# Kernel tuning notes

Measured on AMD Instinct MI355X. Metric: run time of the kernel, lower is better.

Reference implementation:

```python
import jax, jax.numpy as jnp
import numpy as np

N_NODES = 100000
N_EDGES = 1600000
DIM_IN = 128
DIM_OUT = 128


def setup_inputs() -> dict:
    key = jax.random.key(0)
    k_x, k_e, k_w = jax.random.split(key, 3)
    x = jax.random.normal(k_x, (N_NODES, DIM_IN), dtype=jnp.float32)
    edge_index = jax.random.randint(k_e, (2, N_EDGES), 0, N_NODES, dtype=jnp.int64)
    # Glorot-uniform weight like PyG's GCNConv linear layer, stored [d_in, d_out]
    limit = np.sqrt(6.0 / (DIM_IN + DIM_OUT)).astype(np.float32)
    W = jax.random.uniform(k_w, (DIM_IN, DIM_OUT), dtype=jnp.float32, minval=-limit, maxval=limit)
    return {"x": x, "edge_index": edge_index, "W": W}


def reference(x, edge_index, W):
    # PyG GCNConv (bias=False): out = D^{-1/2} (A + I) D^{-1/2} (x @ W)
    N = x.shape[0]
    x_proj = x @ W  # [N, d_out]
    loop = jnp.arange(N, dtype=edge_index.dtype)
    src = jnp.concatenate([edge_index[0], loop])  # message sources (row)
    dst = jnp.concatenate([edge_index[1], loop])  # aggregation targets (col)
    # degree counted at target nodes (edge weight = 1), incl. self loops
    deg = jax.ops.segment_sum(jnp.ones(src.shape, dtype=x.dtype), dst, num_segments=N)
    dis = jnp.where(deg > 0, jax.lax.rsqrt(deg), 0.0)
    norm = dis[src] * dis[dst]  # [E+N]
    msgs = x_proj[src] * norm[:, None]  # [E+N, d_out] gather + scale
    return jax.ops.segment_sum(msgs, dst, num_segments=N)  # scatter-add
```

## Files before the change

### kernel.cpp

```cpp
#include <hip/hip_runtime.h>
#include <hip/hip_bf16.h>

#define DIM 128
#define PCH 2048

typedef __attribute__((ext_vector_type(8))) short bf16x8;
typedef __attribute__((ext_vector_type(4))) float f32x4;

__device__ __forceinline__ float bfu_lo(unsigned u) { return __uint_as_float(u << 16); }
__device__ __forceinline__ float bfu_hi(unsigned u) { return __uint_as_float(u & 0xffff0000u); }
__device__ __forceinline__ unsigned short f2bf(float f) {
    unsigned u = __float_as_uint(f);
    u += 0x7fffu + ((u >> 16) & 1u);
    return (unsigned short)(u >> 16);
}

__device__ __forceinline__ int edge_at(const void* ei, int idx64, long long pos) {
    return idx64 ? (int)__builtin_nontemporal_load((const long long*)ei + pos)
                 : __builtin_nontemporal_load((const int*)ei + pos);
}

__device__ __forceinline__ int detect_idx64(const void* ei, int E, unsigned* s_or, int* s_flag) {
    const unsigned* ei_w = (const unsigned*)ei;
    int t = threadIdx.x;
    unsigned o = 0;
    int lim = (E < 4096) ? E : 4096;
    for (int k = t; k < lim; k += 256) o |= ei_w[2 * k + 1];
    s_or[t] = o;
    __syncthreads();
    for (int s = 128; s > 0; s >>= 1) {
        if (t < s) s_or[t] |= s_or[t + s];
        __syncthreads();
    }
    if (t == 0) *s_flag = (s_or[0] == 0u) ? 1 : 0;
    __syncthreads();
    return *s_flag;
}

__global__ __launch_bounds__(256) void hist_detect(const void* ei, unsigned* bcnt,
                                                   int* flags, int E, int shift) {
    __shared__ unsigned s_h[512];
    __shared__ unsigned s_or[256];
    __shared__ int s_flag;
    int t = threadIdx.x;
    for (int i = t; i < 512; i += 256) s_h[i] = 0u;
    int idx64 = detect_idx64(ei, E, s_or, &s_flag);
    if (blockIdx.x == 0 && t == 0) flags[0] = idx64;
    long long stride = (long long)gridDim.x * 256;
    for (long long e = (long long)blockIdx.x * 256 + t; e < E; e += stride) {
        int d = edge_at(ei, idx64, (long long)E + e);
        atomicAdd(&s_h[d >> shift], 1u);
    }
    __syncthreads();
    for (int i = t; i < 512; i += 256)
        if (s_h[i]) atomicAdd(&bcnt[i], s_h[i]);
}

__global__ __launch_bounds__(256) void partition(const void* ei, const int* __restrict__ flags,
                                                 const unsigned* __restrict__ bcnt,
                                                 unsigned* bcur0, unsigned* pout,
                                                 int E, int B, int shift) {
    __shared__ unsigned s_hist[512], s_off[512], s_gbase[512], s_pref[512], s_bbase[512];
    __shared__ unsigned wsum[4];
    __shared__ unsigned d_arr[PCH], s_arr[PCH];
    int t = threadIdx.x;
    long long base = (long long)blockIdx.x * PCH;
    for (int i = t; i < 512; i += 256) { s_hist[i] = 0u; s_off[i] = 0u; }
    int idx64 = flags[0];

    {
        unsigned v0 = bcnt[2 * t], v1 = bcnt[2 * t + 1];
        unsigned ps = v0 + v1;
        unsigned s = ps;
        int lane = t & 63;
#pragma unroll
        for (int off = 1; off < 64; off <<= 1) {
            unsigned u = __shfl_up(s, off, 64);
            if (lane >= off) s += u;
        }
        int w = t >> 6;
        if (lane == 63) wsum[w] = s;
        __syncthreads();
        unsigned woff = 0;
        for (int j = 0; j < w; j++) woff += wsum[j];
        unsigned excl = woff + s - ps;
        s_bbase[2 * t] = excl;
        s_bbase[2 * t + 1] = excl + v0;
    }
    __syncthreads();

    int d_[PCH / 256], s_[PCH / 256];
#pragma unroll
    for (int j = 0; j < PCH / 256; j++) {
        long long e = base + j * 256 + t;
        if (e < E) {
            d_[j] = edge_at(ei, idx64, (long long)E + e);
            s_[j] = edge_at(ei, idx64, e);
            atomicAdd(&s_hist[d_[j] >> shift], 1u);
        } else d_[j] = -1;
    }
    __syncthreads();

    {
        unsigned v0 = s_hist[2 * t], v1 = s_hist[2 * t + 1];
        unsigned ps = v0 + v1;
        unsigned s = ps;
        int lane = t & 63;
#pragma unroll
        for (int off = 1; off < 64; off <<= 1) {
            unsigned u = __shfl_up(s, off, 64);
            if (lane >= off) s += u;
        }
        int w = t >> 6;
        if (lane == 63) wsum[w] = s;
        __syncthreads();
        unsigned woff = 0;
        for (int j = 0; j < w; j++) woff += wsum[j];
        unsigned excl = woff + s - ps;
        s_pref[2 * t] = excl;
        s_pref[2 * t + 1] = excl + v0;
    }
    __syncthreads();

    for (int i = t; i < B; i += 256)
        if (s_hist[i]) s_gbase[i] = s_bbase[i] + atomicAdd(&bcur0[i], s_hist[i]);
#pragma unroll
    for (int j = 0; j < PCH / 256; j++)
        if (d_[j] >= 0) {
            int b = d_[j] >> shift;
            unsigned p = s_pref[b] + atomicAdd(&s_off[b], 1u);
            d_arr[p] = (unsigned)d_[j];
            s_arr[p] = (unsigned)s_[j];
        }
    __syncthreads();
    long long rem = (long long)E - base;
    unsigned tot = (rem < PCH) ? (unsigned)rem : (unsigned)PCH;
    unsigned msk = (1u << shift) - 1u;
    for (unsigned i = t; i < tot; i += 256) {
        unsigned d = d_arr[i];
        int b = (int)(d >> shift);
        unsigned packed = ((d & msk) << (32 - shift)) | s_arr[i];
        pout[s_gbase[b] + (i - s_pref[b])] = packed;
    }
}

__global__ __launch_bounds__(256) void build_csr(const unsigned* __restrict__ pairs,
                                                 const unsigned* __restrict__ bcnt,
                                                 unsigned* deg, unsigned* row_start,
                                                 float* dis, int* col_src,
                                                 int N, int shift) {
    __shared__ unsigned cnt[512], cur[512], pref[512];
    __shared__ unsigned s_bb[513];
    __shared__ unsigned wsum[4];
    int b = blockIdx.x, t = threadIdx.x;
    int npb = 1 << shift;
    if (npb > 512) npb = 512;
    int nodeLo = b << shift;
    unsigned smask = (1u << (32 - shift)) - 1u;

    {
        unsigned v0 = bcnt[2 * t], v1 = bcnt[2 * t + 1];
        unsigned ps = v0 + v1;
        unsigned s = ps;
        int lane = t & 63;
#pragma unroll
        for (int off = 1; off < 64; off <<= 1) {
            unsigned u = __shfl_up(s, off, 64);
            if (lane >= off) s += u;
        }
        int w = t >> 6;
        if (lane == 63) wsum[w] = s;
        __syncthreads();
        unsigned woff = 0;
        for (int j = 0; j < w; j++) woff += wsum[j];
        unsigned excl = woff + s - ps;
        s_bb[2 * t] = excl;
        s_bb[2 * t + 1] = excl + v0;
        if (t == 255) s_bb[512] = excl + ps;
    }
    __syncthreads();
    unsigned lo = s_bb[b], hi = s_bb[b + 1];

    for (int i = t; i < npb; i += 256) cnt[i] = 0u;
    __syncthreads();
    for (unsigned e = lo + t; e < hi; e += 256) {
        unsigned p = pairs[e];
        atomicAdd(&cnt[p >> (32 - shift)], 1u);
    }
    __syncthreads();
    unsigned v0 = (2 * t < npb) ? cnt[2 * t] : 0u;
    unsigned v1 = (2 * t + 1 < npb) ? cnt[2 * t + 1] : 0u;
    unsigned ps = v0 + v1;
    unsigned s = ps;
    int lane = t & 63;
#pragma unroll
    for (int off = 1; off < 64; off <<= 1) {
        unsigned u = __shfl_up(s, off, 64);
        if (lane >= off) s += u;
    }
    int w = t >> 6;
    if (lane == 63) wsum[w] = s;
    __syncthreads();
    unsigned woff = 0;
    for (int j = 0; j < w; j++) woff += wsum[j];
    unsigned excl = woff + s - ps;
    if (2 * t < npb) pref[2 * t] = excl;
    if (2 * t + 1 < npb) pref[2 * t + 1] = excl + v0;
    __syncthreads();
    for (int i = t; i < npb; i += 256) {
        int node = nodeLo + i;
        unsigned rs = lo + pref[i];
        if (node < N) {
            unsigned c = cnt[i];
            deg[node] = c;
            row_start[node] = rs;
            dis[node] = rsqrtf((float)c + 1.0f);
        }
        cur[i] = rs;
    }
    __syncthreads();
    for (unsigned e = lo + t; e < hi; e += 256) {
        unsigned p = pairs[e];
        unsigned dlow = p >> (32 - shift);
        unsigned pos = atomicAdd(&cur[dlow], 1u);
        col_src[pos] = (int)(p & smask);
    }
}

__global__ __launch_bounds__(256) void gemm_xw(const float* __restrict__ x,
                                               const float* __restrict__ W,
                                               const float* __restrict__ dis,
                                               unsigned short* __restrict__ xps, int N) {
    __shared__ unsigned short wt[128 * 136];
    int tid = threadIdx.x;
    for (int idx = tid; idx < DIM * DIM; idx += 256) {
        int k = idx >> 7, n = idx & 127;
        wt[n * 136 + k] = f2bf(W[idx]);
    }
    __syncthreads();

    int wv = tid >> 6, lane = tid & 63;
    int l15 = lane & 15, quad = lane >> 4;
    int rowBase = blockIdx.x * 128 + wv * 32;

    f32x4 acc[2][8];
#pragma unroll
    for (int mt = 0; mt < 2; mt++)
#pragma unroll
        for (int nt = 0; nt < 8; nt++)
            acc[mt][nt] = (f32x4){0.f, 0.f, 0.f, 0.f};

#pragma unroll
    for (int k0 = 0; k0 < DIM; k0 += 32) {
        bf16x8 aa[2], bb[8];
#pragma unroll
        for (int mt = 0; mt < 2; mt++) {
            int r = rowBase + mt * 16 + l15;
            if (r > N - 1) r = N - 1;
            const float* xf = x + (size_t)r * DIM + k0 + quad * 8;
            float4 u0 = ((const float4*)xf)[0];
            float4 u1 = ((const float4*)xf)[1];
            bf16x8 a;
            a[0] = (short)f2bf(u0.x); a[1] = (short)f2bf(u0.y);
            a[2] = (short)f2bf(u0.z); a[3] = (short)f2bf(u0.w);
            a[4] = (short)f2bf(u1.x); a[5] = (short)f2bf(u1.y);
            a[6] = (short)f2bf(u1.z); a[7] = (short)f2bf(u1.w);
            aa[mt] = a;
        }
#pragma unroll
        for (int nt = 0; nt < 8; nt++)
            bb[nt] = *(const bf16x8*)(wt + (nt * 16 + l15) * 136 + k0 + quad * 8);
#pragma unroll
        for (int mt = 0; mt < 2; mt++)
#pragma unroll
            for (int nt = 0; nt < 8; nt++)
                acc[mt][nt] = __builtin_amdgcn_mfma_f32_16x16x32_bf16(bb[nt], aa[mt], acc[mt][nt], 0, 0, 0);
    }

#pragma unroll
    for (int mt = 0; mt < 2; mt++) {
        int r = rowBase + mt * 16 + l15;
        if (r < N) {
            float sc = dis[r];
#pragma unroll
            for (int nt = 0; nt < 8; nt++) {
                int c0 = nt * 16 + quad * 4;
                ushort4 o;
                o.x = f2bf(acc[mt][nt][0] * sc);
                o.y = f2bf(acc[mt][nt][1] * sc);
                o.z = f2bf(acc[mt][nt][2] * sc);
                o.w = f2bf(acc[mt][nt][3] * sc);
                *(ushort4*)(xps + (size_t)r * DIM + c0) = o;
            }
        }
    }
}

__global__ __launch_bounds__(256) void aggregate(const unsigned short* __restrict__ xps,
                                                 const unsigned* __restrict__ row_start,
                                                 const unsigned* __restrict__ deg,
                                                 const float* __restrict__ dis,
                                                 const int* __restrict__ col_src,
                                                 float* __restrict__ out, int N) {
    int wid = (int)((blockIdx.x * 256 + threadIdx.x) >> 6);
    if (wid >= N) return;
    int lane = threadIdx.x & 63;
    int grp = lane >> 4, lin = lane & 15;
    const uint4* xp4 = (const uint4*)xps;

    float acc[8];
#pragma unroll
    for (int j = 0; j < 8; j++) acc[j] = 0.f;

    unsigned rs = row_start[wid];
    unsigned cnt = deg[wid];
    unsigned tot = cnt + 1;

    for (unsigned base = 0; base < tot; base += 64) {
        unsigned slot = base + (unsigned)lane;
        int idx = (slot < cnt) ? col_src[rs + slot] : wid;
        unsigned rem = tot - base; if (rem > 64) rem = 64;
        for (unsigned q = 0; q * 8 < rem; q++) {
            unsigned sl0 = q * 8 + (unsigned)grp;
            unsigned sl1 = sl0 + 4;
            int s0 = __shfl(idx, (int)sl0, 64);
            int s1 = __shfl(idx, (int)sl1, 64);
            float m0 = (sl0 < rem) ? 1.f : 0.f;
            float m1 = (sl1 < rem) ? 1.f : 0.f;
            uint4 v0 = xp4[(size_t)s0 * 16 + lin];
            uint4 v1 = xp4[(size_t)s1 * 16 + lin];
            acc[0] = fmaf(bfu_lo(v0.x), m0, acc[0]);
            acc[1] = fmaf(bfu_hi(v0.x), m0, acc[1]);
            acc[2] = fmaf(bfu_lo(v0.y), m0, acc[2]);
            acc[3] = fmaf(bfu_hi(v0.y), m0, acc[3]);
            acc[4] = fmaf(bfu_lo(v0.z), m0, acc[4]);
            acc[5] = fmaf(bfu_hi(v0.z), m0, acc[5]);
            acc[6] = fmaf(bfu_lo(v0.w), m0, acc[6]);
            acc[7] = fmaf(bfu_hi(v0.w), m0, acc[7]);
            acc[0] = fmaf(bfu_lo(v1.x), m1, acc[0]);
            acc[1] = fmaf(bfu_hi(v1.x), m1, acc[1]);
            acc[2] = fmaf(bfu_lo(v1.y), m1, acc[2]);
            acc[3] = fmaf(bfu_hi(v1.y), m1, acc[3]);
            acc[4] = fmaf(bfu_lo(v1.z), m1, acc[4]);
            acc[5] = fmaf(bfu_hi(v1.z), m1, acc[5]);
            acc[6] = fmaf(bfu_lo(v1.w), m1, acc[6]);
            acc[7] = fmaf(bfu_hi(v1.w), m1, acc[7]);
        }
    }

#pragma unroll
    for (int j = 0; j < 8; j++) {
        acc[j] += __shfl_xor(acc[j], 16, 64);
        acc[j] += __shfl_xor(acc[j], 32, 64);
    }

    float di = dis[wid];
    if (grp < 2) {
        int jb = (grp & 1) * 4;
        float4 o;
        o.x = acc[jb + 0] * di;
        o.y = acc[jb + 1] * di;
        o.z = acc[jb + 2] * di;
        o.w = acc[jb + 3] * di;
        *(float4*)(out + (size_t)wid * DIM + lin * 8 + jb) = o;
    }
}

extern "C" void kernel_launch(void* const* d_in, const int* in_sizes, int n_in,
                              void* d_out, int out_size, void* d_ws, size_t ws_size,
                              hipStream_t stream) {
    const int N = in_sizes[0] / DIM;
    const int E = in_sizes[1] / 2;
    const float* x = (const float*)d_in[0];
    const void* ei = d_in[1];
    const float* W = (const float*)d_in[2];
    float* out = (float*)d_out;

    int shift = 8;
    while ((((long long)N + (1LL << shift) - 1) >> shift) > 512 && shift < 9) shift++;
    int B = (int)(((long long)N + (1LL << shift) - 1) >> shift);

    char* wsp = (char*)d_ws;
    size_t off = 0;
    auto alloc = [&](size_t b) { void* p = wsp + off; off += (b + 255) & ~(size_t)255; return p; };
    unsigned* bcnt       = (unsigned*)alloc(4096);
    unsigned* bcur0      = bcnt + 512;
    int*      flags      = (int*)alloc(256);
    unsigned* deg        = (unsigned*)alloc((size_t)N * 4);
    unsigned* row_start  = (unsigned*)alloc((size_t)N * 4);
    float*    dis        = (float*)alloc((size_t)N * 4);
    int*      col_src    = (int*)alloc((size_t)E * 4);
    unsigned short* xps  = (unsigned short*)alloc((size_t)N * DIM * 2);

    unsigned* pairs = (unsigned*)xps;
    if ((size_t)E * 4 > (size_t)N * DIM * 2 && off + (size_t)E * 4 <= ws_size)
        pairs = (unsigned*)alloc((size_t)E * 4);

    hipMemsetAsync(bcnt, 0, 4096, stream);
    hist_detect<<<512, 256, 0, stream>>>(ei, bcnt, flags, E, shift);
    partition<<<(E + PCH - 1) / PCH, 256, 0, stream>>>(ei, flags, bcnt, bcur0, pairs, E, B, shift);
    build_csr<<<B, 256, 0, stream>>>(pairs, bcnt, deg, row_start, dis, col_src, N, shift);
    gemm_xw<<<(N + 127) / 128, 256, 0, stream>>>(x, W, dis, xps, N);
    aggregate<<<(N + 3) / 4, 256, 0, stream>>>(xps, row_start, deg, dis, col_src, out, N);
}
```

Measured before the change: 244.9 us.

## Switch CSR build to coarse 2048-node partition with fine per-block filtering

The edge partition now bins destinations into 64 coarse buckets of 2048 nodes instead of up to 512 buckets of 256 nodes, with a larger 4096-edge chunk per partition block. This cuts the scattered global writes in partition to few contiguous runs. build_csr then launches one block per 256-node fine bucket; each block scans its whole coarse bucket (8x redundant reads of pairs), keeps only its own edges and stages them in LDS before scattering into col_src, falling back to a rescan if more than 8192 match. The packing hardcodes 21 bits for the source id, so it assumes N is below 2^21.

```diff
diff --git a/kernel.cpp b/kernel.cpp
--- a/kernel.cpp
+++ b/kernel.cpp
@@ -2,7 +2,11 @@
 #include <hip/hip_bf16.h>
 
 #define DIM 128
-#define PCH 2048
+#define PCH 4096
+#define CAP 8192
+#define SHIFT_F 8
+#define SHIFT_C 11
+#define FPC 8
 
 typedef __attribute__((ext_vector_type(8))) short bf16x8;
 typedef __attribute__((ext_vector_type(4))) float f32x4;
@@ -38,54 +42,43 @@
 }
 
 __global__ __launch_bounds__(256) void hist_detect(const void* ei, unsigned* bcnt,
-                                                   int* flags, int E, int shift) {
-    __shared__ unsigned s_h[512];
+                                                   int* flags, int E) {
+    __shared__ unsigned s_h[64];
     __shared__ unsigned s_or[256];
     __shared__ int s_flag;
     int t = threadIdx.x;
-    for (int i = t; i < 512; i += 256) s_h[i] = 0u;
+    if (t < 64) s_h[t] = 0u;
     int idx64 = detect_idx64(ei, E, s_or, &s_flag);
     if (blockIdx.x == 0 && t == 0) flags[0] = idx64;
     long long stride = (long long)gridDim.x * 256;
     for (long long e = (long long)blockIdx.x * 256 + t; e < E; e += stride) {
         int d = edge_at(ei, idx64, (long long)E + e);
-        atomicAdd(&s_h[d >> shift], 1u);
-    }
-    __syncthreads();
-    for (int i = t; i < 512; i += 256)
-        if (s_h[i]) atomicAdd(&bcnt[i], s_h[i]);
+        atomicAdd(&s_h[d >> SHIFT_C], 1u);
+    }
+    __syncthreads();
+    if (t < 64 && s_h[t]) atomicAdd(&bcnt[t], s_h[t]);
 }
 
 __global__ __launch_bounds__(256) void partition(const void* ei, const int* __restrict__ flags,
                                                  const unsigned* __restrict__ bcnt,
                                                  unsigned* bcur0, unsigned* pout,
-                                                 int E, int B, int shift) {
-    __shared__ unsigned s_hist[512], s_off[512], s_gbase[512], s_pref[512], s_bbase[512];
-    __shared__ unsigned wsum[4];
+                                                 int E, int Bc) {
+    __shared__ unsigned s_hist[64], s_off[64], s_gbase[64], s_pref[64], s_bbase[64];
     __shared__ unsigned d_arr[PCH], s_arr[PCH];
     int t = threadIdx.x;
     long long base = (long long)blockIdx.x * PCH;
-    for (int i = t; i < 512; i += 256) { s_hist[i] = 0u; s_off[i] = 0u; }
+    if (t < 64) { s_hist[t] = 0u; s_off[t] = 0u; }
     int idx64 = flags[0];
 
-    {
-        unsigned v0 = bcnt[2 * t], v1 = bcnt[2 * t + 1];
-        unsigned ps = v0 + v1;
-        unsigned s = ps;
-        int lane = t & 63;
+    if (t < 64) {
+        unsigned v = (t < Bc) ? bcnt[t] : 0u;
+        unsigned s = v;
 #pragma unroll
         for (int off = 1; off < 64; off <<= 1) {
             unsigned u = __shfl_up(s, off, 64);
-            if (lane >= off) s += u;
-        }
-        int w = t >> 6;
-        if (lane == 63) wsum[w] = s;
-        __syncthreads();
-        unsigned woff = 0;
-        for (int j = 0; j < w; j++) woff += wsum[j];
-        unsigned excl = woff + s - ps;
-        s_bbase[2 * t] = excl;
-        s_bbase[2 * t + 1] = excl + v0;
+            if (t >= off) s += u;
+        }
+        s_bbase[t] = s - v;
     }
     __syncthreads();
 
@@ -96,38 +89,29 @@
         if (e < E) {
             d_[j] = edge_at(ei, idx64, (long long)E + e);
             s_[j] = edge_at(ei, idx64, e);
-            atomicAdd(&s_hist[d_[j] >> shift], 1u);
+            atomicAdd(&s_hist[d_[j] >> SHIFT_C], 1u);
         } else d_[j] = -1;
     }
     __syncthreads();
 
-    {
-        unsigned v0 = s_hist[2 * t], v1 = s_hist[2 * t + 1];
-        unsigned ps = v0 + v1;
-        unsigned s = ps;
-        int lane = t & 63;
+    if (t < 64) {
+        unsigned v = s_hist[t];
+        unsigned s = v;
 #pragma unroll
         for (int off = 1; off < 64; off <<= 1) {
             unsigned u = __shfl_up(s, off, 64);
-            if (lane >= off) s += u;
-        }
-        int w = t >> 6;
-        if (lane == 63) wsum[w] = s;
-        __syncthreads();
-        unsigned woff = 0;
-        for (int j = 0; j < w; j++) woff += wsum[j];
-        unsigned excl = woff + s - ps;
-        s_pref[2 * t] = excl;
-        s_pref[2 * t + 1] = excl + v0;
-    }
-    __syncthreads();
-
-    for (int i = t; i < B; i += 256)
-        if (s_hist[i]) s_gbase[i] = s_bbase[i] + atomicAdd(&bcur0[i], s_hist[i]);
+            if (t >= off) s += u;
+        }
+        s_pref[t] = s - v;
+    }
+    __syncthreads();
+
+    if (t < Bc && s_hist[t])
+        s_gbase[t] = s_bbase[t] + atomicAdd(&bcur0[t], s_hist[t]);
 #pragma unroll
     for (int j = 0; j < PCH / 256; j++)
         if (d_[j] >= 0) {
-            int b = d_[j] >> shift;
+            int b = d_[j] >> SHIFT_C;
             unsigned p = s_pref[b] + atomicAdd(&s_off[b], 1u);
             d_arr[p] = (unsigned)d_[j];
             s_arr[p] = (unsigned)s_[j];
@@ -135,12 +119,12 @@
     __syncthreads();
     long long rem = (long long)E - base;
     unsigned tot = (rem < PCH) ? (unsigned)rem : (unsigned)PCH;
-    unsigned msk = (1u << shift) - 1u;
+    unsigned msk = (1u << SHIFT_C) - 1u;
     for (unsigned i = t; i < tot; i += 256) {
         unsigned d = d_arr[i];
-        int b = (int)(d >> shift);
-        unsigned packed = ((d & msk) << (32 - shift)) | s_arr[i];
-        pout[s_gbase[b] + (i - s_pref[b])] = packed;
+        int b = (int)(d >> SHIFT_C);
+        unsigned pk = ((d & msk) << 21) | s_arr[i];
+        pout[s_gbase[b] + (i - s_pref[b])] = pk;
     }
 }
 
@@ -148,51 +132,61 @@
                                                  const unsigned* __restrict__ bcnt,
                                                  unsigned* deg, unsigned* row_start,
                                                  float* dis, int* col_src,
-                                                 int N, int shift) {
-    __shared__ unsigned cnt[512], cur[512], pref[512];
-    __shared__ unsigned s_bb[513];
+                                                 int N, int Bc) {
+    __shared__ unsigned cnt[256], cur[256], pref[256];
+    __shared__ unsigned s_cb[65];
+    __shared__ unsigned s_sib[FPC];
+    __shared__ unsigned s_scnt;
+    __shared__ unsigned stage[CAP];
     __shared__ unsigned wsum[4];
     int b = blockIdx.x, t = threadIdx.x;
-    int npb = 1 << shift;
-    if (npb > 512) npb = 512;
-    int nodeLo = b << shift;
-    unsigned smask = (1u << (32 - shift)) - 1u;
-
-    {
-        unsigned v0 = bcnt[2 * t], v1 = bcnt[2 * t + 1];
-        unsigned ps = v0 + v1;
-        unsigned s = ps;
-        int lane = t & 63;
+    int g = b >> 3, myfine = b & (FPC - 1);
+    int lane = t & 63;
+
+    if (t < 64) {
+        unsigned v = (t < Bc) ? bcnt[t] : 0u;
+        unsigned s = v;
 #pragma unroll
         for (int off = 1; off < 64; off <<= 1) {
             unsigned u = __shfl_up(s, off, 64);
-            if (lane >= off) s += u;
-        }
-        int w = t >> 6;
-        if (lane == 63) wsum[w] = s;
-        __syncthreads();
-        unsigned woff = 0;
-        for (int j = 0; j < w; j++) woff += wsum[j];
-        unsigned excl = woff + s - ps;
-        s_bb[2 * t] = excl;
-        s_bb[2 * t + 1] = excl + v0;
-        if (t == 255) s_bb[512] = excl + ps;
-    }
-    __syncthreads();
-    unsigned lo = s_bb[b], hi = s_bb[b + 1];
-
-    for (int i = t; i < npb; i += 256) cnt[i] = 0u;
-    __syncthreads();
-    for (unsigned e = lo + t; e < hi; e += 256) {
-        unsigned p = pairs[e];
-        atomicAdd(&cnt[p >> (32 - shift)], 1u);
-    }
-    __syncthreads();
-    unsigned v0 = (2 * t < npb) ? cnt[2 * t] : 0u;
-    unsigned v1 = (2 * t + 1 < npb) ? cnt[2 * t + 1] : 0u;
-    unsigned ps = v0 + v1;
-    unsigned s = ps;
-    int lane = t & 63;
+            if (t >= off) s += u;
+        }
+        s_cb[t] = s - v;
+        if (t == 63) s_cb[64] = s;
+    }
+    cnt[t] = 0u;
+    if (t < FPC) s_sib[t] = 0u;
+    if (t == 0) s_scnt = 0u;
+    __syncthreads();
+    unsigned lo = s_cb[g], hi = (g + 1 < 64) ? s_cb[g + 1] : s_cb[64];
+
+    unsigned iters = (hi - lo + 255u) >> 8;
+    for (unsigned it = 0; it < iters; ++it) {
+        unsigned e = lo + it * 256u + (unsigned)t;
+        bool valid = e < hi;
+        unsigned p = valid ? pairs[e] : 0u;
+        unsigned dlow = p >> 21;
+        int sib = (int)(dlow >> SHIFT_F);
+        bool keep = valid && (sib == myfine);
+        if (valid) atomicAdd(&s_sib[sib], 1u);
+        if (keep) atomicAdd(&cnt[dlow & 255u], 1u);
+        unsigned long long mask = __ballot(keep);
+        if (mask) {
+            int leader = (int)__ffsll((long long)mask) - 1;
+            int rank = (int)__popcll(mask & ((1ull << lane) - 1ull));
+            unsigned basew = 0;
+            if (lane == leader) basew = atomicAdd(&s_scnt, (unsigned)__popcll(mask));
+            basew = (unsigned)__shfl((int)basew, leader, 64);
+            if (keep && basew + (unsigned)rank < CAP) stage[basew + rank] = p;
+        }
+    }
+    __syncthreads();
+
+    unsigned fbase = lo;
+    for (int j = 0; j < myfine; j++) fbase += s_sib[j];
+
+    unsigned v = cnt[t];
+    unsigned s = v;
 #pragma unroll
     for (int off = 1; off < 64; off <<= 1) {
         unsigned u = __shfl_up(s, off, 64);
@@ -203,27 +197,37 @@
     __syncthreads();
     unsigned woff = 0;
     for (int j = 0; j < w; j++) woff += wsum[j];
-    unsigned excl = woff + s - ps;
-    if (2 * t < npb) pref[2 * t] = excl;
-    if (2 * t + 1 < npb) pref[2 * t + 1] = excl + v0;
-    __syncthreads();
-    for (int i = t; i < npb; i += 256) {
-        int node = nodeLo + i;
-        unsigned rs = lo + pref[i];
-        if (node < N) {
-            unsigned c = cnt[i];
-            deg[node] = c;
-            row_start[node] = rs;
-            dis[node] = rsqrtf((float)c + 1.0f);
-        }
-        cur[i] = rs;
-    }
-    __syncthreads();
-    for (unsigned e = lo + t; e < hi; e += 256) {
-        unsigned p = pairs[e];
-        unsigned dlow = p >> (32 - shift);
-        unsigned pos = atomicAdd(&cur[dlow], 1u);
-        col_src[pos] = (int)(p & smask);
+    pref[t] = woff + s - v;
+    __syncthreads();
+
+    int node = (b << SHIFT_F) + t;
+    unsigned rs = fbase + pref[t];
+    if (node < N) {
+        unsigned c = cnt[t];
+        deg[node] = c;
+        row_start[node] = rs;
+        dis[node] = rsqrtf((float)c + 1.0f);
+    }
+    cur[t] = rs;
+    __syncthreads();
+
+    unsigned total = s_scnt;
+    if (total <= CAP) {
+        for (unsigned k = t; k < total; k += 256) {
+            unsigned p = stage[k];
+            unsigned n8 = (p >> 21) & 255u;
+            unsigned pos = atomicAdd(&cur[n8], 1u);
+            col_src[pos] = (int)(p & 0x1FFFFFu);
+        }
+    } else {
+        for (unsigned e = lo + t; e < hi; e += 256) {
+            unsigned p = pairs[e];
+            unsigned dlow = p >> 21;
+            if ((int)(dlow >> SHIFT_F) == myfine) {
+                unsigned pos = atomicAdd(&cur[dlow & 255u], 1u);
+                col_src[pos] = (int)(p & 0x1FFFFFu);
+            }
+        }
     }
 }
 
@@ -376,9 +380,8 @@
     const float* W = (const float*)d_in[2];
     float* out = (float*)d_out;
 
-    int shift = 8;
-    while ((((long long)N + (1LL << shift) - 1) >> shift) > 512 && shift < 9) shift++;
-    int B = (int)(((long long)N + (1LL << shift) - 1) >> shift);
+    int Bc = (N + (1 << SHIFT_C) - 1) >> SHIFT_C;
+    int Bf = (N + (1 << SHIFT_F) - 1) >> SHIFT_F;
 
     char* wsp = (char*)d_ws;
     size_t off = 0;
@@ -397,9 +400,9 @@
         pairs = (unsigned*)alloc((size_t)E * 4);
 
     hipMemsetAsync(bcnt, 0, 4096, stream);
-    hist_detect<<<512, 256, 0, stream>>>(ei, bcnt, flags, E, shift);
-    partition<<<(E + PCH - 1) / PCH, 256, 0, stream>>>(ei, flags, bcnt, bcur0, pairs, E, B, shift);
-    build_csr<<<B, 256, 0, stream>>>(pairs, bcnt, deg, row_start, dis, col_src, N, shift);
+    hist_detect<<<512, 256, 0, stream>>>(ei, bcnt, flags, E);
+    partition<<<(E + PCH - 1) / PCH, 256, 0, stream>>>(ei, flags, bcnt, bcur0, pairs, E, Bc);
+    build_csr<<<Bf, 256, 0, stream>>>(pairs, bcnt, deg, row_start, dis, col_src, N, Bc);
     gemm_xw<<<(N + 127) / 128, 256, 0, stream>>>(x, W, dis, xps, N);
     aggregate<<<(N + 3) / 4, 256, 0, stream>>>(xps, row_start, deg, dis, col_src, out, N);
 }
```

Result: slower. 293.2 us (+19.8%).

## Split edge bucketing into two-pass radix partition with coarse then fine buckets

Applied to the files above, without the earlier changes.

Replaces the single-pass 391-bucket partition with a two-level radix sort: first into 49 coarse buckets of 2048 nodes, then each coarse range is refined into 256-node fine buckets. The aim is to improve write locality of the scatter, since fewer buckets per pass gives longer contiguous runs per block. This adds a full extra read and write pass over the edge array plus an extra kernel launch and more workspace. The node and bucket sizes are now hardcoded constants, so N is assumed to fit those limits (source in 21 bits).

```diff
diff --git a/kernel.cpp b/kernel.cpp
--- a/kernel.cpp
+++ b/kernel.cpp
@@ -2,7 +2,10 @@
 #include <hip/hip_bf16.h>
 
 #define DIM 128
-#define PCH 2048
+#define PCH1 4096
+#define PCH2 2048
+#define SHIFT_C 11
+#define SHIFT_F 8
 
 typedef __attribute__((ext_vector_type(8))) short bf16x8;
 typedef __attribute__((ext_vector_type(4))) float f32x4;
@@ -38,7 +41,7 @@
 }
 
 __global__ __launch_bounds__(256) void hist_detect(const void* ei, unsigned* bcnt,
-                                                   int* flags, int E, int shift) {
+                                                   int* flags, int E) {
     __shared__ unsigned s_h[512];
     __shared__ unsigned s_or[256];
     __shared__ int s_flag;
@@ -49,25 +52,108 @@
     long long stride = (long long)gridDim.x * 256;
     for (long long e = (long long)blockIdx.x * 256 + t; e < E; e += stride) {
         int d = edge_at(ei, idx64, (long long)E + e);
-        atomicAdd(&s_h[d >> shift], 1u);
+        atomicAdd(&s_h[d >> SHIFT_F], 1u);
     }
     __syncthreads();
     for (int i = t; i < 512; i += 256)
         if (s_h[i]) atomicAdd(&bcnt[i], s_h[i]);
 }
 
-__global__ __launch_bounds__(256) void partition(const void* ei, const int* __restrict__ flags,
-                                                 const unsigned* __restrict__ bcnt,
-                                                 unsigned* bcur0, unsigned* pout,
-                                                 int E, int B, int shift) {
-    __shared__ unsigned s_hist[512], s_off[512], s_gbase[512], s_pref[512], s_bbase[512];
+__global__ __launch_bounds__(256) void partition1(const void* ei, const int* __restrict__ flags,
+                                                  const unsigned* __restrict__ bcnt,
+                                                  unsigned* bcur_c, unsigned* pout, int E) {
+    __shared__ unsigned s_hist[64], s_off[64], s_gbase[64], s_pref[64], s_cbase[64];
+    __shared__ unsigned d_arr[PCH1], s_arr[PCH1];
+    int t = threadIdx.x;
+    long long base = (long long)blockIdx.x * PCH1;
+    if (t < 64) { s_hist[t] = 0u; s_off[t] = 0u; }
+    int idx64 = flags[0];
+
+    if (t < 64) {
+        unsigned v = 0;
+#pragma unroll
+        for (int j = 0; j < 8; j++) v += bcnt[t * 8 + j];
+        unsigned s = v;
+#pragma unroll
+        for (int off = 1; off < 64; off <<= 1) {
+            unsigned u = __shfl_up(s, off, 64);
+            if (t >= off) s += u;
+        }
+        s_cbase[t] = s - v;
+    }
+    __syncthreads();
+
+    int d_[PCH1 / 256], s_[PCH1 / 256];
+#pragma unroll
+    for (int j = 0; j < PCH1 / 256; j++) {
+        long long e = base + j * 256 + t;
+        if (e < E) {
+            d_[j] = edge_at(ei, idx64, (long long)E + e);
+            s_[j] = edge_at(ei, idx64, e);
+            atomicAdd(&s_hist[d_[j] >> SHIFT_C], 1u);
+        } else d_[j] = -1;
+    }
+    __syncthreads();
+
+    if (t < 64) {
+        unsigned v = s_hist[t];
+        unsigned s = v;
+#pragma unroll
+        for (int off = 1; off < 64; off <<= 1) {
+            unsigned u = __shfl_up(s, off, 64);
+            if (t >= off) s += u;
+        }
+        s_pref[t] = s - v;
+    }
+    __syncthreads();
+
+    if (t < 64 && s_hist[t])
+        s_gbase[t] = s_cbase[t] + atomicAdd(&bcur_c[t], s_hist[t]);
+#pragma unroll
+    for (int j = 0; j < PCH1 / 256; j++)
+        if (d_[j] >= 0) {
+            int b = d_[j] >> SHIFT_C;
+            unsigned p = s_pref[b] + atomicAdd(&s_off[b], 1u);
+            d_arr[p] = (unsigned)d_[j];
+            s_arr[p] = (unsigned)s_[j];
+        }
+    __syncthreads();
+    long long rem = (long long)E - base;
+    unsigned tot = (rem < PCH1) ? (unsigned)rem : (unsigned)PCH1;
+    unsigned msk = (1u << SHIFT_C) - 1u;
+    for (unsigned i = t; i < tot; i += 256) {
+        unsigned d = d_arr[i];
+        int b = (int)(d >> SHIFT_C);
+        pout[s_gbase[b] + (i - s_pref[b])] = ((d & msk) << 21) | s_arr[i];
+    }
+}
+
+__global__ __launch_bounds__(256) void partition2(const unsigned* __restrict__ pin,
+                                                  const unsigned* __restrict__ bcnt,
+                                                  unsigned* bcur_f, unsigned* pout, int E) {
+    __shared__ unsigned s_cb[65];
+    __shared__ unsigned s_fb[512];
+    __shared__ unsigned s_hist[512], s_off[512], s_gbase[512], s_pref[512];
     __shared__ unsigned wsum[4];
-    __shared__ unsigned d_arr[PCH], s_arr[PCH];
+    __shared__ unsigned pk[PCH2];
+    __shared__ unsigned short f9[PCH2];
     int t = threadIdx.x;
-    long long base = (long long)blockIdx.x * PCH;
+    long long base = (long long)blockIdx.x * PCH2;
     for (int i = t; i < 512; i += 256) { s_hist[i] = 0u; s_off[i] = 0u; }
-    int idx64 = flags[0];
-
+
+    if (t < 64) {
+        unsigned v = 0;
+#pragma unroll
+        for (int j = 0; j < 8; j++) v += bcnt[t * 8 + j];
+        unsigned s = v;
+#pragma unroll
+        for (int off = 1; off < 64; off <<= 1) {
+            unsigned u = __shfl_up(s, off, 64);
+            if (t >= off) s += u;
+        }
+        s_cb[t] = s - v;
+        if (t == 63) s_cb[64] = s;
+    }
     {
         unsigned v0 = bcnt[2 * t], v1 = bcnt[2 * t + 1];
         unsigned ps = v0 + v1;
@@ -84,20 +170,24 @@
         unsigned woff = 0;
         for (int j = 0; j < w; j++) woff += wsum[j];
         unsigned excl = woff + s - ps;
-        s_bbase[2 * t] = excl;
-        s_bbase[2 * t + 1] = excl + v0;
-    }
-    __syncthreads();
-
-    int d_[PCH / 256], s_[PCH / 256];
-#pragma unroll
-    for (int j = 0; j < PCH / 256; j++) {
+        s_fb[2 * t] = excl;
+        s_fb[2 * t + 1] = excl + v0;
+    }
+    __syncthreads();
+
+    unsigned p_[PCH2 / 256];
+    int f_[PCH2 / 256];
+    int c = 0;
+#pragma unroll
+    for (int j = 0; j < PCH2 / 256; j++) {
         long long e = base + j * 256 + t;
         if (e < E) {
-            d_[j] = edge_at(ei, idx64, (long long)E + e);
-            s_[j] = edge_at(ei, idx64, e);
-            atomicAdd(&s_hist[d_[j] >> shift], 1u);
-        } else d_[j] = -1;
+            while (e >= (long long)s_cb[c + 1]) c++;
+            unsigned p = pin[e];
+            p_[j] = p;
+            f_[j] = c * 8 + (int)(p >> 29);
+            atomicAdd(&s_hist[f_[j]], 1u);
+        } else f_[j] = -1;
     }
     __syncthreads();
 
@@ -122,47 +212,38 @@
     }
     __syncthreads();
 
-    for (int i = t; i < B; i += 256)
-        if (s_hist[i]) s_gbase[i] = s_bbase[i] + atomicAdd(&bcur0[i], s_hist[i]);
-#pragma unroll
-    for (int j = 0; j < PCH / 256; j++)
-        if (d_[j] >= 0) {
-            int b = d_[j] >> shift;
-            unsigned p = s_pref[b] + atomicAdd(&s_off[b], 1u);
-            d_arr[p] = (unsigned)d_[j];
-            s_arr[p] = (unsigned)s_[j];
+    for (int i = t; i < 512; i += 256)
+        if (s_hist[i]) s_gbase[i] = s_fb[i] + atomicAdd(&bcur_f[i], s_hist[i]);
+#pragma unroll
+    for (int j = 0; j < PCH2 / 256; j++)
+        if (f_[j] >= 0) {
+            unsigned pp = s_pref[f_[j]] + atomicAdd(&s_off[f_[j]], 1u);
+            pk[pp] = p_[j];
+            f9[pp] = (unsigned short)f_[j];
         }
     __syncthreads();
     long long rem = (long long)E - base;
-    unsigned tot = (rem < PCH) ? (unsigned)rem : (unsigned)PCH;
-    unsigned msk = (1u << shift) - 1u;
+    unsigned tot = (rem < PCH2) ? (unsigned)rem : (unsigned)PCH2;
     for (unsigned i = t; i < tot; i += 256) {
-        unsigned d = d_arr[i];
-        int b = (int)(d >> shift);
-        unsigned packed = ((d & msk) << (32 - shift)) | s_arr[i];
-        pout[s_gbase[b] + (i - s_pref[b])] = packed;
+        int f = f9[i];
+        pout[s_gbase[f] + (i - s_pref[f])] = pk[i];
     }
 }
 
 __global__ __launch_bounds__(256) void build_csr(const unsigned* __restrict__ pairs,
                                                  const unsigned* __restrict__ bcnt,
                                                  unsigned* deg, unsigned* row_start,
-                                                 float* dis, int* col_src,
-                                                 int N, int shift) {
-    __shared__ unsigned cnt[512], cur[512], pref[512];
-    __shared__ unsigned s_bb[513];
+                                                 float* dis, int* col_src, int N) {
+    __shared__ unsigned cnt[256], cur[256], pref2[256];
+    __shared__ unsigned s_fb[513];
     __shared__ unsigned wsum[4];
     int b = blockIdx.x, t = threadIdx.x;
-    int npb = 1 << shift;
-    if (npb > 512) npb = 512;
-    int nodeLo = b << shift;
-    unsigned smask = (1u << (32 - shift)) - 1u;
+    int lane = t & 63;
 
     {
         unsigned v0 = bcnt[2 * t], v1 = bcnt[2 * t + 1];
         unsigned ps = v0 + v1;
         unsigned s = ps;
-        int lane = t & 63;
 #pragma unroll
         for (int off = 1; off < 64; off <<= 1) {
             unsigned u = __shfl_up(s, off, 64);
@@ -174,25 +255,22 @@
         unsigned woff = 0;
         for (int j = 0; j < w; j++) woff += wsum[j];
         unsigned excl = woff + s - ps;
-        s_bb[2 * t] = excl;
-        s_bb[2 * t + 1] = excl + v0;
-        if (t == 255) s_bb[512] = excl + ps;
-    }
-    __syncthreads();
-    unsigned lo = s_bb[b], hi = s_bb[b + 1];
-
-    for (int i = t; i < npb; i += 256) cnt[i] = 0u;
-    __syncthreads();
+        s_fb[2 * t] = excl;
+        s_fb[2 * t + 1] = excl + v0;
+        if (t == 255) s_fb[512] = excl + ps;
+    }
+    cnt[t] = 0u;
+    __syncthreads();
+    unsigned lo = s_fb[b], hi = s_fb[b + 1];
+
     for (unsigned e = lo + t; e < hi; e += 256) {
         unsigned p = pairs[e];
-        atomicAdd(&cnt[p >> (32 - shift)], 1u);
-    }
-    __syncthreads();
-    unsigned v0 = (2 * t < npb) ? cnt[2 * t] : 0u;
-    unsigned v1 = (2 * t + 1 < npb) ? cnt[2 * t + 1] : 0u;
-    unsigned ps = v0 + v1;
-    unsigned s = ps;
-    int lane = t & 63;
+        atomicAdd(&cnt[(p >> 21) & 255u], 1u);
+    }
+    __syncthreads();
+
+    unsigned v = cnt[t];
+    unsigned s = v;
 #pragma unroll
     for (int off = 1; off < 64; off <<= 1) {
         unsigned u = __shfl_up(s, off, 64);
@@ -203,27 +281,23 @@
     __syncthreads();
     unsigned woff = 0;
     for (int j = 0; j < w; j++) woff += wsum[j];
-    unsigned excl = woff + s - ps;
-    if (2 * t < npb) pref[2 * t] = excl;
-    if (2 * t + 1 < npb) pref[2 * t + 1] = excl + v0;
-    __syncthreads();
-    for (int i = t; i < npb; i += 256) {
-        int node = nodeLo + i;
-        unsigned rs = lo + pref[i];
-        if (node < N) {
-            unsigned c = cnt[i];
-            deg[node] = c;
-            row_start[node] = rs;
-            dis[node] = rsqrtf((float)c + 1.0f);
-        }
-        cur[i] = rs;
-    }
+    pref2[t] = woff + s - v;
+    __syncthreads();
+
+    int node = (b << SHIFT_F) + t;
+    unsigned rs = lo + pref2[t];
+    if (node < N) {
+        unsigned c = cnt[t];
+        deg[node] = c;
+        row_start[node] = rs;
+        dis[node] = rsqrtf((float)c + 1.0f);
+    }
+    cur[t] = rs;
     __syncthreads();
     for (unsigned e = lo + t; e < hi; e += 256) {
         unsigned p = pairs[e];
-        unsigned dlow = p >> (32 - shift);
-        unsigned pos = atomicAdd(&cur[dlow], 1u);
-        col_src[pos] = (int)(p & smask);
+        unsigned pos = atomicAdd(&cur[(p >> 21) & 255u], 1u);
+        col_src[pos] = (int)(p & 0x1FFFFFu);
     }
 }
 
@@ -376,30 +450,33 @@
     const float* W = (const float*)d_in[2];
     float* out = (float*)d_out;
 
-    int shift = 8;
-    while ((((long long)N + (1LL << shift) - 1) >> shift) > 512 && shift < 9) shift++;
-    int B = (int)(((long long)N + (1LL << shift) - 1) >> shift);
+    int Bf = (N + (1 << SHIFT_F) - 1) >> SHIFT_F;
 
     char* wsp = (char*)d_ws;
     size_t off = 0;
     auto alloc = [&](size_t b) { void* p = wsp + off; off += (b + 255) & ~(size_t)255; return p; };
-    unsigned* bcnt       = (unsigned*)alloc(4096);
-    unsigned* bcur0      = bcnt + 512;
-    int*      flags      = (int*)alloc(256);
+    unsigned* bcnt   = (unsigned*)alloc(8192);
+    unsigned* bcur_c = bcnt + 512;
+    unsigned* bcur_f = bcnt + 576;
+    int*      flags  = (int*)alloc(256);
     unsigned* deg        = (unsigned*)alloc((size_t)N * 4);
     unsigned* row_start  = (unsigned*)alloc((size_t)N * 4);
     float*    dis        = (float*)alloc((size_t)N * 4);
     int*      col_src    = (int*)alloc((size_t)E * 4);
     unsigned short* xps  = (unsigned short*)alloc((size_t)N * DIM * 2);
 
-    unsigned* pairs = (unsigned*)xps;
-    if ((size_t)E * 4 > (size_t)N * DIM * 2 && off + (size_t)E * 4 <= ws_size)
-        pairs = (unsigned*)alloc((size_t)E * 4);
-
-    hipMemsetAsync(bcnt, 0, 4096, stream);
-    hist_detect<<<512, 256, 0, stream>>>(ei, bcnt, flags, E, shift);
-    partition<<<(E + PCH - 1) / PCH, 256, 0, stream>>>(ei, flags, bcnt, bcur0, pairs, E, B, shift);
-    build_csr<<<B, 256, 0, stream>>>(pairs, bcnt, deg, row_start, dis, col_src, N, shift);
+    unsigned* pout1 = (unsigned*)xps;
+    unsigned* pout2 = pout1 + E;
+    if (off + (size_t)2 * E * 4 <= ws_size) {
+        pout1 = (unsigned*)alloc((size_t)E * 4);
+        pout2 = (unsigned*)alloc((size_t)E * 4);
+    }
+
+    hipMemsetAsync(bcnt, 0, 8192, stream);
+    hist_detect<<<512, 256, 0, stream>>>(ei, bcnt, flags, E);
+    partition1<<<(E + PCH1 - 1) / PCH1, 256, 0, stream>>>(ei, flags, bcnt, bcur_c, pout1, E);
+    partition2<<<(E + PCH2 - 1) / PCH2, 256, 0, stream>>>(pout1, bcnt, bcur_f, pout2, E);
+    build_csr<<<Bf, 256, 0, stream>>>(pout2, bcnt, deg, row_start, dis, col_src, N);
     gemm_xw<<<(N + 127) / 128, 256, 0, stream>>>(x, W, dis, xps, N);
     aggregate<<<(N + 3) / 4, 256, 0, stream>>>(xps, row_start, deg, dis, col_src, out, N);
 }
```

Result: slower. 250.0 us (+2.1%).
